# Performance work log

Measured on AMD Instinct MI355X. Metric: run time of the kernel, lower is better.

The kernel has to match this reference:

```python
import jax, jax.numpy as jnp
import numpy as np

N_LABELS = 48
L = N_LABELS + 2            # labels + stop + start
START = N_LABELS + 1
STOP = N_LABELS
NEG = -10000.0
B, T = 512, 1024


def setup_inputs() -> dict:
    key = jax.random.key(0)
    k1, k2, k3 = jax.random.split(key, 3)
    feats = jax.random.normal(k1, (B, T, L), dtype=jnp.float32)
    lens = jax.random.randint(k2, (B,), 1, T + 1, dtype=jnp.int32)
    transitions = jax.random.normal(k3, (L, L), dtype=jnp.float32)
    return {"feats": feats, "lens": lens, "transitions": transitions}


def reference(feats, lens, transitions):
    # Viterbi decode (module's forward). feats: [B, T, L]
    b, t, l = feats.shape
    vit0 = jnp.full((b, l), NEG, feats.dtype).at[:, START].set(0.0)

    def step(carry, logit):
        vit, c = carry                                   # vit [B,L], c [B]
        scores = vit[:, None, :] + transitions[None, :, :]   # [B, to, from]
        vt_max = scores.max(2)                           # [B, L]
        ptr = scores.argmax(2)                           # [B, L] backpointers
        vit_nxt = vt_max + logit
        vit_new = jnp.where((c > 0)[:, None], vit_nxt, vit)
        # add stop transition exactly when this is the last real timestep
        vit_new = vit_new + jnp.where((c == 1)[:, None], transitions[STOP][None, :], 0.0)
        return (vit_new, c - 1), ptr

    (vit, _), pointers = jax.lax.scan(step, (vit0, lens), jnp.swapaxes(feats, 0, 1))
    scores = vit.max(1)                                  # [B]
    idx = vit.argmax(1)                                  # [B]

    barange = jnp.arange(b)

    def back(i, ptr):
        ni = ptr[barange, i]
        return ni, ni

    _, back_seq = jax.lax.scan(back, idx, pointers, reverse=True)  # back_seq[t] = idx after ptr_t
    # original drops the earliest backtracked index (belongs to the virtual start step)
    paths = jnp.concatenate([back_seq[1:], idx[None]], axis=0).T   # [B, T]
    return scores, paths
```

## Files before the change

kernel.cpp:

```cpp
#include <hip/hip_runtime.h>

typedef unsigned char u8;

#define TT 1024
#define BB 512
#define LL 50
#define STOPI 48
#define STARTI 49
#define NEGV -10000.0f

#define PDW(TO, T4) (((TO) << 8) + ((T4) ^ ((TO) & 31)))
#define PBYTE(S, T) ((((S) << 10) + (((((T) >> 2) ^ ((S) & 31))) << 2)) + ((T) & 3))

#define MAX50(S, M)                                                            \
    {                                                                          \
        float r0_[17];                                                         \
        _Pragma("unroll")                                                      \
        for (int k_ = 0; k_ < 16; ++k_)                                        \
            r0_[k_] = fmaxf(fmaxf((S)[3*k_], (S)[3*k_+1]), (S)[3*k_+2]);       \
        r0_[16] = fmaxf((S)[48], (S)[49]);                                     \
        float r1_[6];                                                          \
        _Pragma("unroll")                                                      \
        for (int k_ = 0; k_ < 5; ++k_)                                         \
            r1_[k_] = fmaxf(fmaxf(r0_[3*k_], r0_[3*k_+1]), r0_[3*k_+2]);       \
        r1_[5] = fmaxf(r0_[15], r0_[16]);                                      \
        (M) = fmaxf(fmaxf(fmaxf(r1_[0], r1_[1]), r1_[2]),                      \
                    fmaxf(fmaxf(r1_[3], r1_[4]), r1_[5]));                     \
    }

#define ROW_ADDS(ROWP, S)                                                      \
    {                                                                          \
        _Pragma("unroll")                                                      \
        for (int k_ = 0; k_ < 13; ++k_) {                                      \
            const float4 q_ = *(const float4*)((ROWP) + 4 * k_);               \
            const int j_ = 4 * k_;                                             \
            (S)[j_ + 0] = q_.x + trr[j_ + 0];                                  \
            (S)[j_ + 1] = q_.y + trr[j_ + 1];                                  \
            if (j_ + 2 < LL) (S)[j_ + 2] = q_.z + trr[j_ + 2];                 \
            if (j_ + 3 < LL) (S)[j_ + 3] = q_.w + trr[j_ + 3];                 \
        }                                                                      \
    }

#define ROWIDX(T, IOUT)                                                        \
    {                                                                          \
        const float* rowp_ = &ring[(T) & 15][0];                               \
        float a_[LL];                                                          \
        ROW_ADDS(rowp_, a_)                                                    \
        float m_; MAX50(a_, m_)                                                \
        int ii_ = 0;                                                           \
        _Pragma("unroll")                                                      \
        for (int j_ = LL - 1; j_ >= 0; --j_)                                   \
            if (a_[j_] == m_) ii_ = j_;                                        \
        (IOUT) = ii_;                                                          \
    }

#define PROCESS_GROUP(BASE)                                                    \
    {                                                                          \
        unsigned pk_ = 0;                                                      \
        _Pragma("unroll 1")                                                    \
        for (int r_ = 0; r_ < 4; ++r_) {                                       \
            const int t_ = (BASE) + r_;                                        \
            int idx_;                                                          \
            if (t_ <= len) {                                                   \
                ROWIDX(t_, idx_)                                               \
            } else {                                                           \
                if (!have) { ROWIDX(len, cidx) have = true; }                  \
                idx_ = cidx;                                                   \
            }                                                                  \
            pk_ |= (unsigned)idx_ << (8 * r_);                                 \
        }                                                                      \
        if (lane < LL)                                                         \
            ((unsigned*)lptr)[PDW(row, (BASE) >> 2)] = pk_;                    \
    }

__global__ __launch_bounds__(192, 2) void viterbi_all(
    const float* __restrict__ feats, const int* __restrict__ lens,
    const float* __restrict__ trans, float* __restrict__ out)
{
    const int b    = blockIdx.x;
    const int tid  = threadIdx.x;
    const int lane = tid & 63;
    const int w    = __builtin_amdgcn_readfirstlane(tid >> 6);
    const int row  = (lane < LL) ? lane : (LL - 1);

    __shared__ float ring[16][64];
    __shared__ u8    lptr[TT * LL];
    __shared__ u8    maps[32 * LL];
    __shared__ int   entries[33];
    __shared__ int   fidx;

    float trr[LL];
#pragma unroll
    for (int j = 0; j < LL; ++j) trr[j] = trans[row * LL + j];
#pragma unroll
    for (int j = 0; j < LL; ++j) asm("" : "+v"(trr[j]));

    const int len  = lens[b];
    const int nit0 = (len >> 3) + 1;
    const int nit  = nit0 > 128 ? 128 : nit0;

    if (w == 0) {
        __builtin_amdgcn_s_setprio(1);
        const float tr_stop = trans[STOPI * LL + row];
        float vit = (lane == STARTI) ? 0.0f : NEGV;
        const float* fb = feats + (size_t)b * (TT * LL);

        float f[8];
#pragma unroll
        for (int i = 0; i < 8; ++i) f[i] = fb[i * LL + row];

        for (int it = 0; it < nit; ++it) {
#pragma unroll
            for (int i = 0; i < 8; ++i) {
                const int t = (it << 3) + i;
                if (t <= len) {
                    if (lane < LL) ring[t & 15][lane] = vit;
                }
                if (t < len) {
                    float a[LL];
#pragma unroll
                    for (int j = 0; j < LL; ++j)
                        a[j] = __int_as_float(__builtin_amdgcn_readlane(
                                   __float_as_int(vit), j)) + trr[j];
                    float m; MAX50(a, m)
                    float nv = m + f[i];
                    if (t == len - 1) nv += tr_stop;
                    vit = nv;
                    int tp = t + 8; if (tp > TT - 1) tp = TT - 1;
                    f[i] = fb[(size_t)tp * LL + row];
                }
            }
            asm volatile("s_waitcnt lgkmcnt(0)" ::: "memory");
            __builtin_amdgcn_s_barrier();
            asm volatile("" ::: "memory");
        }
        __builtin_amdgcn_s_setprio(0);

        float m = -3.4e38f; int mi = 0;
#pragma unroll
        for (int j = 0; j < LL; ++j) {
            float sv = __int_as_float(__builtin_amdgcn_readlane(__float_as_int(vit), j));
            if (sv > m) { m = sv; mi = j; }
        }
        if (lane == 0) { out[b] = m; fidx = mi; }
    } else {
        int  cidx = 0;
        bool have = false;

        for (int it = 0; it < nit; ++it) {
            if (it > 0) {
                const int base = ((it - 1) << 3) + ((w - 1) << 2);
                PROCESS_GROUP(base)
            }
            asm volatile("s_waitcnt lgkmcnt(0)" ::: "memory");
            __builtin_amdgcn_s_barrier();
            asm volatile("" ::: "memory");
        }

        const int base0 = (nit - 1) << 3;
        PROCESS_GROUP(base0 + ((w - 1) << 2))

        const int t0f = base0 + 8;
        if (t0f < TT) {
            if (!have) { ROWIDX(len, cidx) have = true; }
            if (lane < LL) {
                const unsigned pat = (unsigned)cidx * 0x01010101u;
                int tq = t0f;
                if (tq & 8) {
                    if (w == 1) {
                        ((unsigned*)lptr)[PDW(row, tq >> 2)]     = pat;
                        ((unsigned*)lptr)[PDW(row, (tq >> 2)+1)] = pat;
                    }
                    tq += 8;
                }
                for (int t4 = (tq >> 2) + (w - 1) * 4; t4 < 256; t4 += 8) {
                    ((unsigned*)lptr)[PDW(row, t4 + 0)] = pat;
                    ((unsigned*)lptr)[PDW(row, t4 + 1)] = pat;
                    ((unsigned*)lptr)[PDW(row, t4 + 2)] = pat;
                    ((unsigned*)lptr)[PDW(row, t4 + 3)] = pat;
                }
            }
        }
    }

    __syncthreads();

    {
        int st[9], ttt[9], ci[9];
#pragma unroll
        for (int k = 0; k < 9; ++k) {
            int id = tid + 192 * k;
            int valid = id < 1600;
            int idc = valid ? id : 1599;
            int c = idc / 50;
            int l = idc - c * 50;
            st[k] = l; ttt[k] = c * 32 + 31; ci[k] = valid ? idc : -1;
        }
        for (int j = 0; j < 32; ++j) {
#pragma unroll
            for (int k = 0; k < 9; ++k) {
                st[k] = lptr[PBYTE(st[k], ttt[k])];
                ttt[k] -= 1;
            }
        }
#pragma unroll
        for (int k = 0; k < 9; ++k)
            if (ci[k] >= 0) maps[ci[k]] = (u8)st[k];
    }
    __syncthreads();

    const int idx = fidx;

    if (tid == 0) {
        int i = idx;
        for (int c = 31; c >= 0; --c) {
            entries[c + 1] = i;
            i = maps[c * 50 + i];
        }
        entries[0] = i;
    }
    __syncthreads();

    float* po = out + BB + (size_t)b * TT;
    if (tid < 32) {
        const int c = tid;
        int s = entries[c + 1];
        for (int j = 0; j < 32; ++j) {
            int t = c * 32 + 31 - j;
            int ni = lptr[PBYTE(s, t)];
            if (t > 0) po[t - 1] = (float)ni;
            s = ni;
        }
    }
    if (tid == 0) po[TT - 1] = (float)idx;
}

extern "C" void kernel_launch(void* const* d_in, const int* in_sizes, int n_in,
                              void* d_out, int out_size, void* d_ws, size_t ws_size,
                              hipStream_t stream) {
    const float* feats = (const float*)d_in[0];
    const int*   lens  = (const int*)d_in[1];
    const float* trans = (const float*)d_in[2];

    viterbi_all<<<BB, 192, 0, stream>>>(feats, lens, trans, (float*)d_out);
}
```

Before: 562.5 us.

## Publish row maxima to shared ring and spread argmax over four helper waves

The forward wave now also writes each step's max score into a shared ring. Helper waves can then find the backpointer with an equality scan instead of recomputing the 50-way max tree. The block grows from 192 to 320 threads, giving four helper waves that each handle two timesteps per iteration, and the fill loop and map-building loop are re-split to match. This cuts helper-wave work per iteration so it fits under the serial forward recurrence. In exchange it adds one extra LDS store per step on the critical wave and raises register and occupancy pressure.

```diff
diff --git a/kernel.cpp b/kernel.cpp
--- a/kernel.cpp
+++ b/kernel.cpp
@@ -1,6 +1,7 @@
 #include <hip/hip_runtime.h>
 
 typedef unsigned char u8;
+typedef unsigned short u16;
 
 #define TT 1024
 #define BB 512
@@ -28,24 +29,42 @@
                     fmaxf(fmaxf(r1_[3], r1_[4]), r1_[5]));                     \
     }
 
-#define ROW_ADDS(ROWP, S)                                                      \
-    {                                                                          \
+#define FASTIDX(T, IOUT)                                                       \
+    {                                                                          \
+        const float  m_    = mring[(T) & 15][lane];                            \
+        const float* rowp_ = &ring[(T) & 15][0];                               \
+        int ia_ = 63, ib_ = 63, ic_ = 63, id_ = 63;                            \
         _Pragma("unroll")                                                      \
         for (int k_ = 0; k_ < 13; ++k_) {                                      \
-            const float4 q_ = *(const float4*)((ROWP) + 4 * k_);               \
+            const float4 q_ = *(const float4*)(rowp_ + 4 * k_);                \
             const int j_ = 4 * k_;                                             \
-            (S)[j_ + 0] = q_.x + trr[j_ + 0];                                  \
-            (S)[j_ + 1] = q_.y + trr[j_ + 1];                                  \
-            if (j_ + 2 < LL) (S)[j_ + 2] = q_.z + trr[j_ + 2];                 \
-            if (j_ + 3 < LL) (S)[j_ + 3] = q_.w + trr[j_ + 3];                 \
+            { float a_ = q_.x + trr[j_+0]; int c_ = (a_==m_) ? (j_+0) : 63;    \
+              ia_ = c_ < ia_ ? c_ : ia_; }                                     \
+            { float a_ = q_.y + trr[j_+1]; int c_ = (a_==m_) ? (j_+1) : 63;    \
+              ib_ = c_ < ib_ ? c_ : ib_; }                                     \
+            if (j_+2 < LL) { float a_ = q_.z + trr[j_+2];                      \
+              int c_ = (a_==m_) ? (j_+2) : 63; ic_ = c_ < ic_ ? c_ : ic_; }    \
+            if (j_+3 < LL) { float a_ = q_.w + trr[j_+3];                      \
+              int c_ = (a_==m_) ? (j_+3) : 63; id_ = c_ < id_ ? c_ : id_; }    \
         }                                                                      \
-    }
-
-#define ROWIDX(T, IOUT)                                                        \
+        const int m0_ = ia_ < ib_ ? ia_ : ib_;                                 \
+        const int m1_ = ic_ < id_ ? ic_ : id_;                                 \
+        (IOUT) = m0_ < m1_ ? m0_ : m1_;                                        \
+    }
+
+#define TREEIDX(T, IOUT)                                                       \
     {                                                                          \
         const float* rowp_ = &ring[(T) & 15][0];                               \
         float a_[LL];                                                          \
-        ROW_ADDS(rowp_, a_)                                                    \
+        _Pragma("unroll")                                                      \
+        for (int k_ = 0; k_ < 13; ++k_) {                                      \
+            const float4 q_ = *(const float4*)(rowp_ + 4 * k_);                \
+            const int j_ = 4 * k_;                                             \
+            a_[j_+0] = q_.x + trr[j_+0];                                       \
+            a_[j_+1] = q_.y + trr[j_+1];                                       \
+            if (j_+2 < LL) a_[j_+2] = q_.z + trr[j_+2];                        \
+            if (j_+3 < LL) a_[j_+3] = q_.w + trr[j_+3];                        \
+        }                                                                      \
         float m_; MAX50(a_, m_)                                                \
         int ii_ = 0;                                                           \
         _Pragma("unroll")                                                      \
@@ -54,26 +73,29 @@
         (IOUT) = ii_;                                                          \
     }
 
-#define PROCESS_GROUP(BASE)                                                    \
-    {                                                                          \
-        unsigned pk_ = 0;                                                      \
-        _Pragma("unroll 1")                                                    \
-        for (int r_ = 0; r_ < 4; ++r_) {                                       \
-            const int t_ = (BASE) + r_;                                        \
-            int idx_;                                                          \
-            if (t_ <= len) {                                                   \
-                ROWIDX(t_, idx_)                                               \
-            } else {                                                           \
-                if (!have) { ROWIDX(len, cidx) have = true; }                  \
-                idx_ = cidx;                                                   \
-            }                                                                  \
-            pk_ |= (unsigned)idx_ << (8 * r_);                                 \
-        }                                                                      \
+#define PAIR_FAST(B0)                                                          \
+    {                                                                          \
+        int i0_, i1_;                                                          \
+        FASTIDX((B0),     i0_)                                                 \
+        FASTIDX((B0) + 1, i1_)                                                 \
         if (lane < LL)                                                         \
-            ((unsigned*)lptr)[PDW(row, (BASE) >> 2)] = pk_;                    \
-    }
-
-__global__ __launch_bounds__(192, 2) void viterbi_all(
+            *(u16*)(lptr + PBYTE(row, (B0))) = (u16)(i0_ | (i1_ << 8));        \
+    }
+
+#define PAIR_MIXED(B0)                                                         \
+    {                                                                          \
+        int i0_, i1_;                                                          \
+        { const int t_ = (B0);                                                 \
+          if (t_ < len) { FASTIDX(t_, i0_) }                                   \
+          else { if (!have) { TREEIDX(len, cidx) have = true; } i0_ = cidx; } }\
+        { const int t_ = (B0) + 1;                                             \
+          if (t_ < len) { FASTIDX(t_, i1_) }                                   \
+          else { if (!have) { TREEIDX(len, cidx) have = true; } i1_ = cidx; } }\
+        if (lane < LL)                                                         \
+            *(u16*)(lptr + PBYTE(row, (B0))) = (u16)(i0_ | (i1_ << 8));        \
+    }
+
+__global__ __launch_bounds__(320, 2) void viterbi_all(
     const float* __restrict__ feats, const int* __restrict__ lens,
     const float* __restrict__ trans, float* __restrict__ out)
 {
@@ -84,6 +106,7 @@
     const int row  = (lane < LL) ? lane : (LL - 1);
 
     __shared__ float ring[16][64];
+    __shared__ float mring[16][64];
     __shared__ u8    lptr[TT * LL];
     __shared__ u8    maps[32 * LL];
     __shared__ int   entries[33];
@@ -123,6 +146,7 @@
                         a[j] = __int_as_float(__builtin_amdgcn_readlane(
                                    __float_as_int(vit), j)) + trr[j];
                     float m; MAX50(a, m)
+                    if (lane < LL) mring[t & 15][lane] = m;
                     float nv = m + f[i];
                     if (t == len - 1) nv += tr_stop;
                     vit = nv;
@@ -146,39 +170,30 @@
     } else {
         int  cidx = 0;
         bool have = false;
+        const int k0 = (w - 1) << 1;
 
         for (int it = 0; it < nit; ++it) {
             if (it > 0) {
-                const int base = ((it - 1) << 3) + ((w - 1) << 2);
-                PROCESS_GROUP(base)
+                const int base = ((it - 1) << 3) + k0;
+                PAIR_FAST(base)
             }
             asm volatile("s_waitcnt lgkmcnt(0)" ::: "memory");
             __builtin_amdgcn_s_barrier();
             asm volatile("" ::: "memory");
         }
 
-        const int base0 = (nit - 1) << 3;
-        PROCESS_GROUP(base0 + ((w - 1) << 2))
-
-        const int t0f = base0 + 8;
+        {
+            const int base = ((nit - 1) << 3) + k0;
+            PAIR_MIXED(base)
+        }
+
+        const int t0f = nit << 3;
         if (t0f < TT) {
-            if (!have) { ROWIDX(len, cidx) have = true; }
+            if (!have) { TREEIDX(len, cidx) have = true; }
             if (lane < LL) {
                 const unsigned pat = (unsigned)cidx * 0x01010101u;
-                int tq = t0f;
-                if (tq & 8) {
-                    if (w == 1) {
-                        ((unsigned*)lptr)[PDW(row, tq >> 2)]     = pat;
-                        ((unsigned*)lptr)[PDW(row, (tq >> 2)+1)] = pat;
-                    }
-                    tq += 8;
-                }
-                for (int t4 = (tq >> 2) + (w - 1) * 4; t4 < 256; t4 += 8) {
-                    ((unsigned*)lptr)[PDW(row, t4 + 0)] = pat;
-                    ((unsigned*)lptr)[PDW(row, t4 + 1)] = pat;
-                    ((unsigned*)lptr)[PDW(row, t4 + 2)] = pat;
-                    ((unsigned*)lptr)[PDW(row, t4 + 3)] = pat;
-                }
+                for (int t4 = (t0f >> 2) + (w - 1); t4 < 256; t4 += 4)
+                    ((unsigned*)lptr)[PDW(row, t4)] = pat;
             }
         }
     }
@@ -186,26 +201,23 @@
     __syncthreads();
 
     {
-        int st[9], ttt[9], ci[9];
-#pragma unroll
-        for (int k = 0; k < 9; ++k) {
-            int id = tid + 192 * k;
-            int valid = id < 1600;
-            int idc = valid ? id : 1599;
-            int c = idc / 50;
-            int l = idc - c * 50;
-            st[k] = l; ttt[k] = c * 32 + 31; ci[k] = valid ? idc : -1;
+        int st[5], ttt[5], ci[5];
+#pragma unroll
+        for (int k = 0; k < 5; ++k) {
+            const int id = tid + 320 * k;
+            const int c = id / 50;
+            const int l = id - c * 50;
+            st[k] = l; ttt[k] = c * 32 + 31; ci[k] = id;
         }
         for (int j = 0; j < 32; ++j) {
 #pragma unroll
-            for (int k = 0; k < 9; ++k) {
+            for (int k = 0; k < 5; ++k) {
                 st[k] = lptr[PBYTE(st[k], ttt[k])];
                 ttt[k] -= 1;
             }
         }
 #pragma unroll
-        for (int k = 0; k < 9; ++k)
-            if (ci[k] >= 0) maps[ci[k]] = (u8)st[k];
+        for (int k = 0; k < 5; ++k) maps[ci[k]] = (u8)st[k];
     }
     __syncthreads();
 
@@ -242,5 +254,5 @@
     const int*   lens  = (const int*)d_in[1];
     const float* trans = (const float*)d_in[2];
 
-    viterbi_all<<<BB, 192, 0, stream>>>(feats, lens, trans, (float*)d_out);
+    viterbi_all<<<BB, 320, 0, stream>>>(feats, lens, trans, (float*)d_out);
 }
```

Result: slower. 939.5 us (+67.0%).
